# Optimization experiments

Hardware: AMD Instinct MI355X
Metric: run time of the kernel (lower is better)

The kernel has to match this reference:

```python
import jax, jax.numpy as jnp
import numpy as np

C_IN = 64
C_HIDDEN = 8
NO_HEADS = 8
INF = 1.0e9
EPS_ATT = 1.0e-10
LN_EPS = 1.0e-5
N_SEQ = 2048
N_RES = 384


def setup_inputs() -> dict:
    key = jax.random.key(0)
    ks = jax.random.split(key, 8)
    HC = NO_HEADS * C_HIDDEN
    m = jax.random.normal(ks[0], (N_SEQ, N_RES, C_IN), dtype=jnp.float32)
    mask = jnp.ones((N_SEQ, N_RES), dtype=jnp.float32)
    s = 0.05
    return {
        "m": m,
        "mask": mask,
        "ln_w": jnp.ones((C_IN,), jnp.float32),
        "ln_b": jnp.zeros((C_IN,), jnp.float32),
        "wq": jax.random.normal(ks[1], (C_IN, HC), jnp.float32) * s,
        "wk": jax.random.normal(ks[2], (C_IN, C_HIDDEN), jnp.float32) * s,
        "wv": jax.random.normal(ks[3], (C_IN, C_HIDDEN), jnp.float32) * s,
        "wg": jax.random.normal(ks[4], (C_IN, HC), jnp.float32) * s,
        "bg": jnp.ones((HC,), jnp.float32),  # gating bias init = 1
        "wo": jax.random.normal(ks[5], (HC, C_IN), jnp.float32) * s,
        "bo": jnp.zeros((C_IN,), jnp.float32),
    }


def reference(m, mask, ln_w, ln_b, wq, wk, wv, wg, bg, wo, bo):
    H, Ch = NO_HEADS, C_HIDDEN
    # transpose: m -> [R, S, C], mask -> [R, S]
    mt = jnp.swapaxes(m, -2, -3)
    mk = jnp.swapaxes(mask, -1, -2)
    # LayerNorm over c_in (population variance, as torch)
    mu = jnp.mean(mt, axis=-1, keepdims=True)
    var = jnp.mean(jnp.square(mt - mu), axis=-1, keepdims=True)
    x = (mt - mu) * jax.lax.rsqrt(var + LN_EPS) * ln_w + ln_b  # [R, S, C]
    # mean-pooled global query over the sequence (MSA depth) dim
    q = jnp.sum(x * mk[..., None], axis=-2) / (jnp.sum(mk, axis=-1)[..., None] + EPS_ATT)  # [R, C]
    q = (q @ wq) * (Ch ** -0.5)
    q = q.reshape(q.shape[:-1] + (H, Ch))  # [R, H, Ch]
    k = x @ wk  # [R, S, Ch] (shared across heads)
    v = x @ wv  # [R, S, Ch]
    a = jnp.einsum("rhc,rsc->rhs", q, k) + (INF * (mk - 1.0))[..., None, :]
    a = jax.nn.softmax(a, axis=-1)  # [R, H, S]
    o = jnp.einsum("rhs,rsc->rhc", a, v)  # [R, H, Ch]
    g = jax.nn.sigmoid(x @ wg + bg).reshape(x.shape[:-1] + (H, Ch))  # [R, S, H, Ch]
    o = o[..., None, :, :] * g  # [R, S, H, Ch]
    o = o.reshape(o.shape[:-2] + (H * Ch,))
    out = o @ wo + bo  # [R, S, C]
    return jnp.swapaxes(out, -2, -3)  # back to [S, R, C]
```

## Files before the change

### kernel.cpp

```cpp
#include <hip/hip_runtime.h>
#include <hip/hip_bf16.h>

#define S_SEQ 2048
#define R_RES 384
#define CIN   64
#define HC    64
#define NH    8
#define CHD   8

using bf16x8 = __attribute__((ext_vector_type(8))) short;
using f32x4  = __attribute__((ext_vector_type(4))) float;

__device__ __forceinline__ short f2bf(float v) {
  __hip_bfloat16 h = __float2bfloat16(v);
  union { __hip_bfloat16 b; short s; } u; u.b = h; return u.s;
}
__device__ __forceinline__ float bf2f(short s) {
  union { short s; __hip_bfloat16 b; } u; u.s = s; return __bfloat162float(u.b);
}

__global__ __launch_bounds__(256) void k0_prep(
    const float* __restrict__ wg, const float* __restrict__ wo,
    const float* __restrict__ wk, const float* __restrict__ wv,
    const float* __restrict__ ln_w, const float* __restrict__ ln_b,
    short* __restrict__ wgT_hi, short* __restrict__ wgT_lo,
    short* __restrict__ woT_hi, short* __restrict__ woT_lo,
    short* __restrict__ wkvT_hi, short* __restrict__ wkvT_lo,
    float* __restrict__ bkv) {
  const int idx = blockIdx.x * 256 + threadIdx.x;
  if (idx < 16) {
    float s = 0.f;
    for (int c = 0; c < CIN; ++c)
      s += ln_b[c] * ((idx < 8) ? wk[c * CHD + idx] : wv[c * CHD + (idx - 8)]);
    bkv[idx] = s;
  }
  if (idx < 16 * CIN) {
    const int a = idx >> 6, c = idx & 63;
    const float w = ln_w[c] * ((a < 8) ? wk[c * CHD + a] : wv[c * CHD + (a - 8)]);
    short h = f2bf(w);
    wkvT_hi[idx] = h; wkvT_lo[idx] = f2bf(w - bf2f(h));
  }
  if (idx >= HC * CIN) return;
  const int a = idx >> 6;
  const int b = idx & 63;
  const float g = wg[b * HC + a];
  short gh = f2bf(g);
  wgT_hi[idx] = gh; wgT_lo[idx] = f2bf(g - bf2f(gh));
  const float o = wo[b * CIN + a];
  short oh = f2bf(o);
  woT_hi[idx] = oh; woT_lo[idx] = f2bf(o - bf2f(oh));
}

__global__ __launch_bounds__(256, 4) void k1_mfma(
    const float* __restrict__ m, const float* __restrict__ mask,
    const short* __restrict__ wkvT_hi, const short* __restrict__ wkvT_lo,
    const float* __restrict__ bkv,
    float* __restrict__ Kd, float* __restrict__ Vd,
    float* __restrict__ qpool_part, float* __restrict__ qm_part) {
  const int r = blockIdx.x;
  const int chunk = blockIdx.y;
  const int tid = threadIdx.x;
  const int wave = tid >> 6;
  const int lane = tid & 63;
  const int lrow = lane & 15;
  const int lpart = lane >> 4;
  const int s_base = chunk * 512 + wave * 128;

  __shared__ float redA[4][CIN];
  __shared__ float redM[4];

  bf16x8 kvh[2], kvl[2];
  #pragma unroll
  for (int k = 0; k < 2; ++k) {
    const int idx = lrow * 64 + k * 32 + lpart * 8;
    kvh[k] = *reinterpret_cast<const bf16x8*>(wkvT_hi + idx);
    kvl[k] = *reinterpret_cast<const bf16x8*>(wkvT_lo + idx);
  }
  const float4 bkvq = *reinterpret_cast<const float4*>(bkv + lpart * 4);

  float qacc[16];
  #pragma unroll
  for (int e = 0; e < 16; ++e) qacc[e] = 0.f;
  float macc = 0.f;

  for (int t = 0; t < 8; ++t) {
    const int srow = s_base + t * 16 + lrow;
    const float* mrow = m + ((size_t)srow * R_RES + r) * CIN;
    float x0[8], x1[8];
    {
      const float4* p0 = reinterpret_cast<const float4*>(mrow + lpart * 8);
      const float4* p1 = reinterpret_cast<const float4*>(mrow + 32 + lpart * 8);
      float4 a = p0[0], b = p0[1], c = p1[0], d = p1[1];
      x0[0]=a.x; x0[1]=a.y; x0[2]=a.z; x0[3]=a.w; x0[4]=b.x; x0[5]=b.y; x0[6]=b.z; x0[7]=b.w;
      x1[0]=c.x; x1[1]=c.y; x1[2]=c.z; x1[3]=c.w; x1[4]=d.x; x1[5]=d.y; x1[6]=d.z; x1[7]=d.w;
    }
    const float mk = mask[(size_t)srow * R_RES + r];

    float s = 0.f;
    #pragma unroll
    for (int e = 0; e < 8; ++e) s += x0[e] + x1[e];
    s += __shfl_xor(s, 16, 64);
    s += __shfl_xor(s, 32, 64);
    const float mean = s * (1.0f / CIN);
    float vs = 0.f;
    #pragma unroll
    for (int e = 0; e < 8; ++e) {
      float d0 = x0[e] - mean, d1 = x1[e] - mean;
      vs += d0 * d0 + d1 * d1;
    }
    vs += __shfl_xor(vs, 16, 64);
    vs += __shfl_xor(vs, 32, 64);
    const float rstd = rsqrtf(vs * (1.0f / CIN) + 1e-5f);

    bf16x8 ah0, al0, ah1, al1;
    #pragma unroll
    for (int e = 0; e < 8; ++e) {
      const float xh0 = (x0[e] - mean) * rstd;
      const float xh1 = (x1[e] - mean) * rstd;
      qacc[e]     += mk * xh0;
      qacc[8 + e] += mk * xh1;
      short h = f2bf(xh0);
      ah0[e] = h; al0[e] = f2bf(xh0 - bf2f(h));
      h = f2bf(xh1);
      ah1[e] = h; al1[e] = f2bf(xh1 - bf2f(h));
    }
    macc += mk;

    f32x4 a = {0.f, 0.f, 0.f, 0.f};
    a = __builtin_amdgcn_mfma_f32_16x16x32_bf16(kvh[0], ah0, a, 0, 0, 0);
    a = __builtin_amdgcn_mfma_f32_16x16x32_bf16(kvh[1], ah1, a, 0, 0, 0);
    a = __builtin_amdgcn_mfma_f32_16x16x32_bf16(kvl[0], ah0, a, 0, 0, 0);
    a = __builtin_amdgcn_mfma_f32_16x16x32_bf16(kvl[1], ah1, a, 0, 0, 0);
    a = __builtin_amdgcn_mfma_f32_16x16x32_bf16(kvh[0], al0, a, 0, 0, 0);
    a = __builtin_amdgcn_mfma_f32_16x16x32_bf16(kvh[1], al1, a, 0, 0, 0);

    const size_t off = ((size_t)r * S_SEQ + srow) * CHD + (lpart & 1) * 4;
    float* dst = ((lpart & 2) ? Vd : Kd) + off;
    *reinterpret_cast<float4*>(dst) =
        make_float4(a[0] + bkvq.x, a[1] + bkvq.y, a[2] + bkvq.z, a[3] + bkvq.w);
  }

  #pragma unroll
  for (int off = 1; off <= 8; off <<= 1) {
    #pragma unroll
    for (int e = 0; e < 16; ++e) qacc[e] += __shfl_xor(qacc[e], off, 64);
    macc += __shfl_xor(macc, off, 64);
  }
  if (lrow == 0) {
    #pragma unroll
    for (int e = 0; e < 8; ++e) {
      redA[wave][lpart * 8 + e] = qacc[e];
      redA[wave][32 + lpart * 8 + e] = qacc[8 + e];
    }
    if (lpart == 0) redM[wave] = macc;
  }
  __syncthreads();
  if (tid < CIN) {
    const float tot = redA[0][tid] + redA[1][tid] + redA[2][tid] + redA[3][tid];
    qpool_part[((size_t)chunk * R_RES + r) * CIN + tid] = tot;
  }
  if (tid == 0)
    qm_part[chunk * R_RES + r] = redM[0] + redM[1] + redM[2] + redM[3];
}

__global__ __launch_bounds__(256) void k2_attn(
    const float* __restrict__ mask,
    const float* __restrict__ ln_w, const float* __restrict__ ln_b,
    const float* __restrict__ wq,
    const float* __restrict__ qpool_part, const float* __restrict__ qm_part,
    const float* __restrict__ Kd, const float* __restrict__ Vd,
    float* __restrict__ od) {
  const int r = blockIdx.x;
  const int tid = threadIdx.x;
  const int lane = tid & 63;
  const int wave = tid >> 6;

  __shared__ float s_q[HC];
  __shared__ float s_qp[CIN];
  __shared__ float redw[4][CIN];
  __shared__ float dred[4][NH];
  __shared__ float mred[4][NH];

  const float msum_tot = qm_part[0 * R_RES + r] + qm_part[1 * R_RES + r] +
                         qm_part[2 * R_RES + r] + qm_part[3 * R_RES + r];

  if (tid < CIN) {
    float A = 0.f;
    #pragma unroll
    for (int ch = 0; ch < 4; ++ch)
      A += qpool_part[((size_t)ch * R_RES + r) * CIN + tid];
    s_qp[tid] = (ln_w[tid] * A + ln_b[tid] * msum_tot) / (msum_tot + 1e-10f);
  }
  __syncthreads();
  if (tid < HC) {
    float qj = 0.f;
    for (int c = 0; c < CIN; ++c) qj += s_qp[c] * wq[c * HC + tid];
    s_q[tid] = qj * 0.35355339059327373f;
  }
  __syncthreads();

  float hmax[NH];
  #pragma unroll
  for (int h = 0; h < NH; ++h) hmax[h] = -1e30f;

  for (int s = tid; s < S_SEQ; s += 256) {
    float kk[CHD];
    const float4* kp = reinterpret_cast<const float4*>(Kd + ((size_t)r * S_SEQ + s) * CHD);
    float4 a = kp[0], b = kp[1];
    kk[0] = a.x; kk[1] = a.y; kk[2] = a.z; kk[3] = a.w;
    kk[4] = b.x; kk[5] = b.y; kk[6] = b.z; kk[7] = b.w;
    const float madd = 1e9f * (mask[(size_t)s * R_RES + r] - 1.0f);
    #pragma unroll
    for (int h = 0; h < NH; ++h) {
      float l = madd;
      #pragma unroll
      for (int j = 0; j < CHD; ++j) l += s_q[h * CHD + j] * kk[j];
      hmax[h] = fmaxf(hmax[h], l);
    }
  }
  #pragma unroll
  for (int h = 0; h < NH; ++h) {
    #pragma unroll
    for (int off = 32; off >= 1; off >>= 1)
      hmax[h] = fmaxf(hmax[h], __shfl_xor(hmax[h], off, 64));
  }
  if (lane == 0) {
    #pragma unroll
    for (int h = 0; h < NH; ++h) mred[wave][h] = hmax[h];
  }
  __syncthreads();
  #pragma unroll
  for (int h = 0; h < NH; ++h)
    hmax[h] = fmaxf(fmaxf(mred[0][h], mred[1][h]), fmaxf(mred[2][h], mred[3][h]));

  float opart[HC];
  #pragma unroll
  for (int i = 0; i < HC; ++i) opart[i] = 0.f;
  float dpart[NH];
  #pragma unroll
  for (int h = 0; h < NH; ++h) dpart[h] = 0.f;

  for (int s = tid; s < S_SEQ; s += 256) {
    float kk[CHD], vv[CHD];
    const float4* kp = reinterpret_cast<const float4*>(Kd + ((size_t)r * S_SEQ + s) * CHD);
    const float4* vp = reinterpret_cast<const float4*>(Vd + ((size_t)r * S_SEQ + s) * CHD);
    float4 a = kp[0], b = kp[1], c4 = vp[0], d4 = vp[1];
    kk[0] = a.x; kk[1] = a.y; kk[2] = a.z; kk[3] = a.w;
    kk[4] = b.x; kk[5] = b.y; kk[6] = b.z; kk[7] = b.w;
    vv[0] = c4.x; vv[1] = c4.y; vv[2] = c4.z; vv[3] = c4.w;
    vv[4] = d4.x; vv[5] = d4.y; vv[6] = d4.z; vv[7] = d4.w;
    const float madd = 1e9f * (mask[(size_t)s * R_RES + r] - 1.0f);
    #pragma unroll
    for (int h = 0; h < NH; ++h) {
      float l = madd;
      #pragma unroll
      for (int j = 0; j < CHD; ++j) l += s_q[h * CHD + j] * kk[j];
      const float p = __expf(l - hmax[h]);
      dpart[h] += p;
      #pragma unroll
      for (int j = 0; j < CHD; ++j) opart[h * CHD + j] += p * vv[j];
    }
  }

  #pragma unroll
  for (int h = 0; h < NH; ++h) {
    float v = dpart[h];
    #pragma unroll
    for (int off = 32; off >= 1; off >>= 1) v += __shfl_xor(v, off, 64);
    dpart[h] = v;
  }
  if (lane == 0) {
    #pragma unroll
    for (int h = 0; h < NH; ++h) dred[wave][h] = dpart[h];
  }
  float keep = 0.f;
  #pragma unroll
  for (int c = 0; c < HC; ++c) {
    float val = opart[c];
    #pragma unroll
    for (int off = 32; off >= 1; off >>= 1) val += __shfl_xor(val, off, 64);
    if (lane == c) keep = val;
  }
  redw[wave][lane] = keep;
  __syncthreads();
  if (tid < HC) {
    const float tot = redw[0][tid] + redw[1][tid] + redw[2][tid] + redw[3][tid];
    const int h = tid >> 3;
    const float den = dred[0][h] + dred[1][h] + dred[2][h] + dred[3][h];
    od[(size_t)r * HC + tid] = tot / den;
  }
}

__global__ __launch_bounds__(128) void k3_mfma(
    const float* __restrict__ m,
    const float* __restrict__ ln_w, const float* __restrict__ ln_b,
    const short* __restrict__ wgT_hi, const short* __restrict__ wgT_lo,
    const short* __restrict__ woT_hi, const short* __restrict__ woT_lo,
    const float* __restrict__ bg, const float* __restrict__ bo,
    const float* __restrict__ od, float* __restrict__ out) {
  const int tid = threadIdx.x;
  const int wave = tid >> 6;
  const int lane = tid & 63;
  const int lrow = lane & 15;
  const int lpart = lane >> 4;
  const size_t base = (size_t)blockIdx.x * 128 + (size_t)wave * 64;
  const int base_r = (int)(base % R_RES);

  __shared__ float t_lds[2][64 * 64];
  float* tw = t_lds[wave];

  float bgv[4], bov[4];
  #pragma unroll
  for (int n = 0; n < 4; ++n) { bgv[n] = bg[n * 16 + lrow]; bov[n] = bo[n * 16 + lrow]; }

  float lw0[8], lb0[8], lw1[8], lb1[8];
  {
    const float4* w0 = reinterpret_cast<const float4*>(ln_w + lpart * 8);
    const float4* w1 = reinterpret_cast<const float4*>(ln_w + 32 + lpart * 8);
    const float4* b0 = reinterpret_cast<const float4*>(ln_b + lpart * 8);
    const float4* b1 = reinterpret_cast<const float4*>(ln_b + 32 + lpart * 8);
    float4 a = w0[0], b = w0[1], c = w1[0], d = w1[1];
    lw0[0]=a.x; lw0[1]=a.y; lw0[2]=a.z; lw0[3]=a.w; lw0[4]=b.x; lw0[5]=b.y; lw0[6]=b.z; lw0[7]=b.w;
    lw1[0]=c.x; lw1[1]=c.y; lw1[2]=c.z; lw1[3]=c.w; lw1[4]=d.x; lw1[5]=d.y; lw1[6]=d.z; lw1[7]=d.w;
    a = b0[0]; b = b0[1]; c = b1[0]; d = b1[1];
    lb0[0]=a.x; lb0[1]=a.y; lb0[2]=a.z; lb0[3]=a.w; lb0[4]=b.x; lb0[5]=b.y; lb0[6]=b.z; lb0[7]=b.w;
    lb1[0]=c.x; lb1[1]=c.y; lb1[2]=c.z; lb1[3]=c.w; lb1[4]=d.x; lb1[5]=d.y; lb1[6]=d.z; lb1[7]=d.w;
  }

  bf16x8 b1h[4][2], b1l[4][2];
  #pragma unroll
  for (int n = 0; n < 4; ++n) {
    #pragma unroll
    for (int k = 0; k < 2; ++k) {
      const int idx = (n * 16 + lrow) * 64 + k * 32 + lpart * 8;
      b1h[n][k] = *reinterpret_cast<const bf16x8*>(wgT_hi + idx);
      b1l[n][k] = *reinterpret_cast<const bf16x8*>(wgT_lo + idx);
    }
  }

  #pragma unroll
  for (int mt = 0; mt < 4; ++mt) {
    const size_t grow = base + mt * 16 + lrow;
    const float* mrow = m + grow * CIN;
    float x0[8], x1[8];
    {
      const float4* p0 = reinterpret_cast<const float4*>(mrow + lpart * 8);
      const float4* p1 = reinterpret_cast<const float4*>(mrow + 32 + lpart * 8);
      float4 a = p0[0], b = p0[1], c = p1[0], d = p1[1];
      x0[0]=a.x; x0[1]=a.y; x0[2]=a.z; x0[3]=a.w; x0[4]=b.x; x0[5]=b.y; x0[6]=b.z; x0[7]=b.w;
      x1[0]=c.x; x1[1]=c.y; x1[2]=c.z; x1[3]=c.w; x1[4]=d.x; x1[5]=d.y; x1[6]=d.z; x1[7]=d.w;
    }
    float s = 0.f;
    #pragma unroll
    for (int e = 0; e < 8; ++e) s += x0[e] + x1[e];
    s += __shfl_xor(s, 16, 64);
    s += __shfl_xor(s, 32, 64);
    const float mean = s * (1.0f / CIN);
    float vs = 0.f;
    #pragma unroll
    for (int e = 0; e < 8; ++e) {
      float d0 = x0[e] - mean, d1 = x1[e] - mean;
      vs += d0 * d0 + d1 * d1;
    }
    vs += __shfl_xor(vs, 16, 64);
    vs += __shfl_xor(vs, 32, 64);
    const float rstd = rsqrtf(vs * (1.0f / CIN) + 1e-5f);

    bf16x8 ah0, al0, ah1, al1;
    #pragma unroll
    for (int e = 0; e < 8; ++e) {
      float xn = (x0[e] - mean) * rstd * lw0[e] + lb0[e];
      short h = f2bf(xn);
      ah0[e] = h; al0[e] = f2bf(xn - bf2f(h));
      xn = (x1[e] - mean) * rstd * lw1[e] + lb1[e];
      h = f2bf(xn);
      ah1[e] = h; al1[e] = f2bf(xn - bf2f(h));
    }

    #pragma unroll
    for (int n = 0; n < 4; ++n) {
      f32x4 acc = {0.f, 0.f, 0.f, 0.f};
      acc = __builtin_amdgcn_mfma_f32_16x16x32_bf16(ah0, b1h[n][0], acc, 0, 0, 0);
      acc = __builtin_amdgcn_mfma_f32_16x16x32_bf16(ah1, b1h[n][1], acc, 0, 0, 0);
      acc = __builtin_amdgcn_mfma_f32_16x16x32_bf16(ah0, b1l[n][0], acc, 0, 0, 0);
      acc = __builtin_amdgcn_mfma_f32_16x16x32_bf16(ah1, b1l[n][1], acc, 0, 0, 0);
      acc = __builtin_amdgcn_mfma_f32_16x16x32_bf16(al0, b1h[n][0], acc, 0, 0, 0);
      acc = __builtin_amdgcn_mfma_f32_16x16x32_bf16(al1, b1h[n][1], acc, 0, 0, 0);
      const int j = n * 16 + lrow;
      #pragma unroll
      for (int i = 0; i < 4; ++i) {
        const int rl = mt * 16 + lpart * 4 + i;
        int r = base_r + rl; if (r >= R_RES) r -= R_RES;
        const float z = acc[i] + bgv[n];
        const float g = 1.0f / (1.0f + __expf(-z));
        const float t = g * od[(size_t)r * HC + j];
        const int off = ((rl * 256 + j * 4)) ^ ((rl & 7) << 4);
        *reinterpret_cast<float*>(reinterpret_cast<char*>(tw) + off) = t;
      }
    }
  }

  __syncthreads();

  bf16x8 b2h[4][2], b2l[4][2];
  #pragma unroll
  for (int n = 0; n < 4; ++n) {
    #pragma unroll
    for (int k = 0; k < 2; ++k) {
      const int idx = (n * 16 + lrow) * 64 + k * 32 + lpart * 8;
      b2h[n][k] = *reinterpret_cast<const bf16x8*>(woT_hi + idx);
      b2l[n][k] = *reinterpret_cast<const bf16x8*>(woT_lo + idx);
    }
  }

  #pragma unroll
  for (int mt = 0; mt < 4; ++mt) {
    const int rl2 = mt * 16 + lrow;
    const int swz = (rl2 & 7) << 4;
    bf16x8 ah0, al0, ah1, al1;
    {
      const int a0 = rl2 * 256 + lpart * 32;
      const int a1 = rl2 * 256 + 128 + lpart * 32;
      char* tb = reinterpret_cast<char*>(tw);
      float4 u0 = *reinterpret_cast<float4*>(tb + (a0 ^ swz));
      float4 u1 = *reinterpret_cast<float4*>(tb + ((a0 + 16) ^ swz));
      float4 u2 = *reinterpret_cast<float4*>(tb + (a1 ^ swz));
      float4 u3 = *reinterpret_cast<float4*>(tb + ((a1 + 16) ^ swz));
      float t0[8] = {u0.x, u0.y, u0.z, u0.w, u1.x, u1.y, u1.z, u1.w};
      float t1[8] = {u2.x, u2.y, u2.z, u2.w, u3.x, u3.y, u3.z, u3.w};
      #pragma unroll
      for (int e = 0; e < 8; ++e) {
        short h = f2bf(t0[e]);
        ah0[e] = h; al0[e] = f2bf(t0[e] - bf2f(h));
        h = f2bf(t1[e]);
        ah1[e] = h; al1[e] = f2bf(t1[e] - bf2f(h));
      }
    }
    #pragma unroll
    for (int n = 0; n < 4; ++n) {
      f32x4 acc = {0.f, 0.f, 0.f, 0.f};
      acc = __builtin_amdgcn_mfma_f32_16x16x32_bf16(ah0, b2h[n][0], acc, 0, 0, 0);
      acc = __builtin_amdgcn_mfma_f32_16x16x32_bf16(ah1, b2h[n][1], acc, 0, 0, 0);
      acc = __builtin_amdgcn_mfma_f32_16x16x32_bf16(ah0, b2l[n][0], acc, 0, 0, 0);
      acc = __builtin_amdgcn_mfma_f32_16x16x32_bf16(ah1, b2l[n][1], acc, 0, 0, 0);
      acc = __builtin_amdgcn_mfma_f32_16x16x32_bf16(al0, b2h[n][0], acc, 0, 0, 0);
      acc = __builtin_amdgcn_mfma_f32_16x16x32_bf16(al1, b2h[n][1], acc, 0, 0, 0);
      const int cc = n * 16 + lrow;
      #pragma unroll
      for (int i = 0; i < 4; ++i) {
        const size_t grow = base + mt * 16 + lpart * 4 + i;
        out[grow * CIN + cc] = acc[i] + bov[n];
      }
    }
  }
}

extern "C" void kernel_launch(void* const* d_in, const int* in_sizes, int n_in,
                              void* d_out, int out_size, void* d_ws, size_t ws_size,
                              hipStream_t stream) {
  const float* m    = (const float*)d_in[0];
  const float* mask = (const float*)d_in[1];
  const float* ln_w = (const float*)d_in[2];
  const float* ln_b = (const float*)d_in[3];
  const float* wq   = (const float*)d_in[4];
  const float* wk   = (const float*)d_in[5];
  const float* wv   = (const float*)d_in[6];
  const float* wg   = (const float*)d_in[7];
  const float* bg   = (const float*)d_in[8];
  const float* wo   = (const float*)d_in[9];
  const float* bo   = (const float*)d_in[10];
  float* out = (float*)d_out;

  const size_t sizeK   = (size_t)R_RES * S_SEQ * CHD * sizeof(float);
  const size_t sizeQP  = (size_t)4 * R_RES * CIN * sizeof(float);
  const size_t sizeQM  = (size_t)4 * R_RES * sizeof(float);
  const size_t sizeO   = (size_t)R_RES * HC * sizeof(float);
  const size_t sizeW   = (size_t)HC * CIN * sizeof(short);
  const size_t sizeWKV = (size_t)16 * CIN * sizeof(short);

  char* ws = (char*)d_ws;
  float* Kd         = (float*)(ws);
  float* Vd         = (float*)(ws + sizeK);
  float* qpool_part = (float*)(ws + 2 * sizeK);
  float* qm_part    = (float*)(ws + 2 * sizeK + sizeQP);
  float* od         = (float*)(ws + 2 * sizeK + sizeQP + sizeQM);
  char* wbase       = ws + 2 * sizeK + sizeQP + sizeQM + sizeO;
  short* wgT_hi  = (short*)(wbase);
  short* wgT_lo  = (short*)(wbase + sizeW);
  short* woT_hi  = (short*)(wbase + 2 * sizeW);
  short* woT_lo  = (short*)(wbase + 3 * sizeW);
  short* wkvT_hi = (short*)(wbase + 4 * sizeW);
  short* wkvT_lo = (short*)(wbase + 4 * sizeW + sizeWKV);
  float* bkv     = (float*)(wbase + 4 * sizeW + 2 * sizeWKV);

  k0_prep<<<(HC * CIN + 255) / 256, 256, 0, stream>>>(
      wg, wo, wk, wv, ln_w, ln_b,
      wgT_hi, wgT_lo, woT_hi, woT_lo, wkvT_hi, wkvT_lo, bkv);

  k1_mfma<<<dim3(R_RES, 4), 256, 0, stream>>>(
      m, mask, wkvT_hi, wkvT_lo, bkv, Kd, Vd, qpool_part, qm_part);

  k2_attn<<<R_RES, 256, 0, stream>>>(
      mask, ln_w, ln_b, wq, qpool_part, qm_part, Kd, Vd, od);

  k3_mfma<<<(S_SEQ * R_RES) / 128, 128, 0, stream>>>(
      m, ln_w, ln_b, wgT_hi, wgT_lo, woT_hi, woT_lo, bg, bo, od, out);
}
```

Baseline: 223.9 us.

## Split attention over sequence chunks with combine kernel and transposed output

The attention kernel is split into four sequence chunks per residue, launched as a 2D grid. Each chunk writes its partial output, denominator and max, and a new combine kernel merges them with log-sum-exp rescaling. The combine kernel writes the attention output transposed (head-channel major), so the gating kernel can fetch four consecutive residues with one float4 load instead of four scalar gathers. This raises the block count for the latency-bound attention stage, at the cost of an extra kernel launch and partial-result traffic.

Result: slower. 246.0 us (+9.9%).

```diff
diff --git a/kernel.cpp b/kernel.cpp
--- a/kernel.cpp
+++ b/kernel.cpp
@@ -163,17 +163,20 @@
     qm_part[chunk * R_RES + r] = redM[0] + redM[1] + redM[2] + redM[3];
 }
 
-__global__ __launch_bounds__(256) void k2_attn(
+__global__ __launch_bounds__(256) void k2a_attn_part(
     const float* __restrict__ mask,
     const float* __restrict__ ln_w, const float* __restrict__ ln_b,
     const float* __restrict__ wq,
     const float* __restrict__ qpool_part, const float* __restrict__ qm_part,
     const float* __restrict__ Kd, const float* __restrict__ Vd,
-    float* __restrict__ od) {
+    float* __restrict__ odp, float* __restrict__ mpart,
+    float* __restrict__ dpart) {
   const int r = blockIdx.x;
+  const int chunk = blockIdx.y;
   const int tid = threadIdx.x;
   const int lane = tid & 63;
   const int wave = tid >> 6;
+  const int s_lo = chunk * 512;
 
   __shared__ float s_q[HC];
   __shared__ float s_qp[CIN];
@@ -203,7 +206,7 @@
   #pragma unroll
   for (int h = 0; h < NH; ++h) hmax[h] = -1e30f;
 
-  for (int s = tid; s < S_SEQ; s += 256) {
+  for (int s = s_lo + tid; s < s_lo + 512; s += 256) {
     float kk[CHD];
     const float4* kp = reinterpret_cast<const float4*>(Kd + ((size_t)r * S_SEQ + s) * CHD);
     float4 a = kp[0], b = kp[1];
@@ -236,11 +239,11 @@
   float opart[HC];
   #pragma unroll
   for (int i = 0; i < HC; ++i) opart[i] = 0.f;
-  float dpart[NH];
-  #pragma unroll
-  for (int h = 0; h < NH; ++h) dpart[h] = 0.f;
-
-  for (int s = tid; s < S_SEQ; s += 256) {
+  float dp[NH];
+  #pragma unroll
+  for (int h = 0; h < NH; ++h) dp[h] = 0.f;
+
+  for (int s = s_lo + tid; s < s_lo + 512; s += 256) {
     float kk[CHD], vv[CHD];
     const float4* kp = reinterpret_cast<const float4*>(Kd + ((size_t)r * S_SEQ + s) * CHD);
     const float4* vp = reinterpret_cast<const float4*>(Vd + ((size_t)r * S_SEQ + s) * CHD);
@@ -256,7 +259,7 @@
       #pragma unroll
       for (int j = 0; j < CHD; ++j) l += s_q[h * CHD + j] * kk[j];
       const float p = __expf(l - hmax[h]);
-      dpart[h] += p;
+      dp[h] += p;
       #pragma unroll
       for (int j = 0; j < CHD; ++j) opart[h * CHD + j] += p * vv[j];
     }
@@ -264,14 +267,14 @@
 
   #pragma unroll
   for (int h = 0; h < NH; ++h) {
-    float v = dpart[h];
+    float v = dp[h];
     #pragma unroll
     for (int off = 32; off >= 1; off >>= 1) v += __shfl_xor(v, off, 64);
-    dpart[h] = v;
+    dp[h] = v;
   }
   if (lane == 0) {
     #pragma unroll
-    for (int h = 0; h < NH; ++h) dred[wave][h] = dpart[h];
+    for (int h = 0; h < NH; ++h) dred[wave][h] = dp[h];
   }
   float keep = 0.f;
   #pragma unroll
@@ -284,11 +287,39 @@
   redw[wave][lane] = keep;
   __syncthreads();
   if (tid < HC) {
-    const float tot = redw[0][tid] + redw[1][tid] + redw[2][tid] + redw[3][tid];
-    const int h = tid >> 3;
-    const float den = dred[0][h] + dred[1][h] + dred[2][h] + dred[3][h];
-    od[(size_t)r * HC + tid] = tot / den;
-  }
+    odp[((size_t)chunk * R_RES + r) * HC + tid] =
+        redw[0][tid] + redw[1][tid] + redw[2][tid] + redw[3][tid];
+  }
+  if (tid < NH) {
+    dpart[((size_t)chunk * R_RES + r) * NH + tid] =
+        dred[0][tid] + dred[1][tid] + dred[2][tid] + dred[3][tid];
+    mpart[((size_t)chunk * R_RES + r) * NH + tid] = hmax[tid];
+  }
+}
+
+__global__ __launch_bounds__(256) void k2b_combine(
+    const float* __restrict__ odp, const float* __restrict__ mpart,
+    const float* __restrict__ dpart, float* __restrict__ odT) {
+  const int tid = threadIdx.x;
+  const int r = blockIdx.x * 4 + (tid >> 6);
+  const int j = tid & 63;
+  const int h = j >> 3;
+  float mc[4], dc[4], oc[4];
+  #pragma unroll
+  for (int c = 0; c < 4; ++c) {
+    mc[c] = mpart[((size_t)c * R_RES + r) * NH + h];
+    dc[c] = dpart[((size_t)c * R_RES + r) * NH + h];
+    oc[c] = odp[((size_t)c * R_RES + r) * HC + j];
+  }
+  const float mstar = fmaxf(fmaxf(mc[0], mc[1]), fmaxf(mc[2], mc[3]));
+  float num = 0.f, den = 0.f;
+  #pragma unroll
+  for (int c = 0; c < 4; ++c) {
+    const float sc = __expf(mc[c] - mstar);
+    num += oc[c] * sc;
+    den += dc[c] * sc;
+  }
+  odT[(size_t)j * R_RES + r] = num / den;
 }
 
 __global__ __launch_bounds__(128) void k3_mfma(
@@ -297,7 +328,7 @@
     const short* __restrict__ wgT_hi, const short* __restrict__ wgT_lo,
     const short* __restrict__ woT_hi, const short* __restrict__ woT_lo,
     const float* __restrict__ bg, const float* __restrict__ bo,
-    const float* __restrict__ od, float* __restrict__ out) {
+    const float* __restrict__ odT, float* __restrict__ out) {
   const int tid = threadIdx.x;
   const int wave = tid >> 6;
   const int lane = tid & 63;
@@ -387,13 +418,15 @@
       acc = __builtin_amdgcn_mfma_f32_16x16x32_bf16(al0, b1h[n][0], acc, 0, 0, 0);
       acc = __builtin_amdgcn_mfma_f32_16x16x32_bf16(al1, b1h[n][1], acc, 0, 0, 0);
       const int j = n * 16 + lrow;
+      const int r0 = base_r + mt * 16 + lpart * 4;
+      const float4 odq = *reinterpret_cast<const float4*>(odT + (size_t)j * R_RES + r0);
+      const float oarr[4] = {odq.x, odq.y, odq.z, odq.w};
       #pragma unroll
       for (int i = 0; i < 4; ++i) {
         const int rl = mt * 16 + lpart * 4 + i;
-        int r = base_r + rl; if (r >= R_RES) r -= R_RES;
         const float z = acc[i] + bgv[n];
         const float g = 1.0f / (1.0f + __expf(-z));
-        const float t = g * od[(size_t)r * HC + j];
+        const float t = g * oarr[i];
         const int off = ((rl * 256 + j * 4)) ^ ((rl & 7) << 4);
         *reinterpret_cast<float*>(reinterpret_cast<char*>(tw) + off) = t;
       }
@@ -474,24 +507,29 @@
   const size_t sizeK   = (size_t)R_RES * S_SEQ * CHD * sizeof(float);
   const size_t sizeQP  = (size_t)4 * R_RES * CIN * sizeof(float);
   const size_t sizeQM  = (size_t)4 * R_RES * sizeof(float);
-  const size_t sizeO   = (size_t)R_RES * HC * sizeof(float);
+  const size_t sizeODP = (size_t)4 * R_RES * HC * sizeof(float);
+  const size_t sizeMP  = (size_t)4 * R_RES * NH * sizeof(float);
+  const size_t sizeODT = (size_t)R_RES * HC * sizeof(float);
   const size_t sizeW   = (size_t)HC * CIN * sizeof(short);
   const size_t sizeWKV = (size_t)16 * CIN * sizeof(short);
 
   char* ws = (char*)d_ws;
   float* Kd         = (float*)(ws);
   float* Vd         = (float*)(ws + sizeK);
-  float* qpool_part = (float*)(ws + 2 * sizeK);
-  float* qm_part    = (float*)(ws + 2 * sizeK + sizeQP);
-  float* od         = (float*)(ws + 2 * sizeK + sizeQP + sizeQM);
-  char* wbase       = ws + 2 * sizeK + sizeQP + sizeQM + sizeO;
-  short* wgT_hi  = (short*)(wbase);
-  short* wgT_lo  = (short*)(wbase + sizeW);
-  short* woT_hi  = (short*)(wbase + 2 * sizeW);
-  short* woT_lo  = (short*)(wbase + 3 * sizeW);
-  short* wkvT_hi = (short*)(wbase + 4 * sizeW);
-  short* wkvT_lo = (short*)(wbase + 4 * sizeW + sizeWKV);
-  float* bkv     = (float*)(wbase + 4 * sizeW + 2 * sizeWKV);
+  char* p           = ws + 2 * sizeK;
+  float* qpool_part = (float*)p;               p += sizeQP;
+  float* qm_part    = (float*)p;               p += sizeQM;
+  float* odp        = (float*)p;               p += sizeODP;
+  float* mpart      = (float*)p;               p += sizeMP;
+  float* dpart      = (float*)p;               p += sizeMP;
+  float* odT        = (float*)p;               p += sizeODT;
+  short* wgT_hi  = (short*)p;                  p += sizeW;
+  short* wgT_lo  = (short*)p;                  p += sizeW;
+  short* woT_hi  = (short*)p;                  p += sizeW;
+  short* woT_lo  = (short*)p;                  p += sizeW;
+  short* wkvT_hi = (short*)p;                  p += sizeWKV;
+  short* wkvT_lo = (short*)p;                  p += sizeWKV;
+  float* bkv     = (float*)p;
 
   k0_prep<<<(HC * CIN + 255) / 256, 256, 0, stream>>>(
       wg, wo, wk, wv, ln_w, ln_b,
@@ -500,9 +538,11 @@
   k1_mfma<<<dim3(R_RES, 4), 256, 0, stream>>>(
       m, mask, wkvT_hi, wkvT_lo, bkv, Kd, Vd, qpool_part, qm_part);
 
-  k2_attn<<<R_RES, 256, 0, stream>>>(
-      mask, ln_w, ln_b, wq, qpool_part, qm_part, Kd, Vd, od);
+  k2a_attn_part<<<dim3(R_RES, 4), 256, 0, stream>>>(
+      mask, ln_w, ln_b, wq, qpool_part, qm_part, Kd, Vd, odp, mpart, dpart);
+
+  k2b_combine<<<R_RES / 4, 256, 0, stream>>>(odp, mpart, dpart, odT);
 
   k3_mfma<<<(S_SEQ * R_RES) / 128, 128, 0, stream>>>(
-      m, ln_w, ln_b, wgT_hi, wgT_lo, woT_hi, woT_lo, bg, bo, od, out);
-}
+      m, ln_w, ln_b, wgT_hi, wgT_lo, woT_hi, woT_lo, bg, bo, odT, out);
+}
```
